# Optimization experiments

Measured on AMD Instinct MI355X. Metric: run time of the kernel, lower is better.

The kernel has to match this reference:

```python
import jax, jax.numpy as jnp
import numpy as np
import math

H = 12          # num_heads
HD = 64         # head_dim
M = 32          # random features = head_dim * kernel_ratio
EPS = 1e-8


def prm_exp(x, w):
    # x: [B,H,T,HD], w: [H,M,HD] -> [B,H,T,M]
    xd = 0.5 * jnp.sum(x * x, axis=-1, keepdims=True)        # [B,H,T,1]
    wtx = jnp.einsum('bhti,hmi->bhtm', x, w)                  # [B,H,T,M]
    return jnp.exp(wtx - xd) / math.sqrt(M)


def setup_inputs() -> dict:
    key = jax.random.key(0)
    ks = jax.random.split(key, 5)
    B, N, C = 8, 4096, 768
    x = jax.random.normal(ks[0], (B, N, C), dtype=jnp.float32)
    kqv_w = jax.random.normal(ks[1], (3 * C, C), dtype=jnp.float32) * (1.0 / math.sqrt(C))
    kqv_b = jnp.zeros((3 * C,), dtype=jnp.float32)
    proj_w = jax.random.normal(ks[2], (C, C), dtype=jnp.float32) * (1.0 / math.sqrt(C))
    proj_b = jnp.zeros((C,), dtype=jnp.float32)
    # frozen random-feature matrix: orthogonal rows per head, scaled by sqrt(M)
    wr = jax.random.normal(ks[3], (H, M, HD), dtype=jnp.float32)
    q_ortho, _ = jnp.linalg.qr(jnp.swapaxes(wr, -1, -2))       # [H,HD,M], cols orthonormal
    w = jnp.swapaxes(q_ortho, -1, -2) * math.sqrt(M)           # [H,M,HD]
    return {"x": x, "kqv_w": kqv_w, "kqv_b": kqv_b,
            "proj_w": proj_w, "proj_b": proj_b, "w": w}


def reference(x, kqv_w, kqv_b, proj_w, proj_b, w):
    B, N, C = x.shape
    kqv = x @ kqv_w.T + kqv_b                                  # [B,N,3C]
    kqv = kqv.reshape(B, N, 3, H, HD).transpose(2, 0, 3, 1, 4) # [3,B,H,N,HD]
    k, q, v = kqv[0], kqv[1], kqv[2]
    kp = prm_exp(k, w)                                         # [B,H,N,M]
    qp = prm_exp(q, w)                                         # [B,H,N,M]
    D = jnp.einsum('bhtm,bhm->bht', qp, kp.sum(axis=2))[..., None]   # [B,H,N,1]
    kptv = jnp.einsum('bhin,bhim->bhnm', v, kp)                # [B,H,HD,M]
    y = jnp.einsum('bhtm,bhnm->bhtn', qp, kptv) / (D + EPS)    # [B,H,N,HD]
    y = y.transpose(0, 2, 1, 3).reshape(B, N, C)
    y = y @ proj_w.T + proj_b
    return y
```

## Files before the change

kernel.cpp:

```cpp
#include <hip/hip_runtime.h>
#include <math.h>

namespace {
constexpr int cB  = 8;
constexpr int cN  = 4096;
constexpr int cC  = 768;
constexpr int cH  = 12;
constexpr int cHD = 64;
constexpr int cM  = 32;
}

typedef __attribute__((ext_vector_type(8))) short bf16x8;
typedef __attribute__((ext_vector_type(4))) float f32x4;

#define BARRIER() do { asm volatile("" ::: "memory"); __builtin_amdgcn_s_barrier(); asm volatile("" ::: "memory"); } while (0)
#define WAIT_VM(N) do { asm volatile("s_waitcnt vmcnt(" #N ")" ::: "memory"); __builtin_amdgcn_sched_barrier(0); } while (0)
#define WAIT_LGKM0() do { asm volatile("s_waitcnt lgkmcnt(0)" ::: "memory"); __builtin_amdgcn_sched_barrier(0); } while (0)

__device__ __forceinline__ void async_copy16(const void* g, void* l) {
    __builtin_amdgcn_global_load_lds((const __attribute__((address_space(1))) void*)g,
                                     (__attribute__((address_space(3))) void*)l, 16, 0, 0);
}

__device__ __forceinline__ ushort f32_to_bf16_rne(float x) {
    unsigned int u = __float_as_uint(x);
    u += 0x7fffu + ((u >> 16) & 1u);
    return (ushort)(u >> 16);
}

__device__ __forceinline__ float bf16_to_f32(ushort u) {
    return __uint_as_float(((unsigned)u) << 16);
}

__device__ __forceinline__ void split2(float f, ushort& h, ushort& l) {
    h = f32_to_bf16_rne(f);
    float r = f - bf16_to_f32(h);
    l = f32_to_bf16_rne(r);
}

__global__ __launch_bounds__(256)
void split_bf16(const float* __restrict__ in, ushort* __restrict__ hi,
                ushort* __restrict__ lo, int n4)
{
    int i = blockIdx.x * 256 + threadIdx.x;
    const int stride = gridDim.x * 256;
    for (; i < n4; i += stride) {
        float4 v = reinterpret_cast<const float4*>(in)[i];
        ushort4 h, l;
        split2(v.x, h.x, l.x);
        split2(v.y, h.y, l.y);
        split2(v.z, h.z, l.z);
        split2(v.w, h.w, l.w);
        reinterpret_cast<ushort4*>(hi)[i] = h;
        reinterpret_cast<ushort4*>(lo)[i] = l;
    }
}

template <int TERMS, int FUSE>
__global__ __launch_bounds__(512, 2)
void gemm256(const ushort* __restrict__ Ah, const ushort* __restrict__ Al,
             const ushort* __restrict__ Bh, const ushort* __restrict__ Bl,
             const float* __restrict__ bias,
             float* __restrict__ Cf, ushort* __restrict__ Cb,
             int Ndim, int K, int mode,
             ushort* __restrict__ kp, ushort* __restrict__ qp,
             float* __restrict__ kpsum_p,
             const ushort* __restrict__ whb, const ushort* __restrict__ wlb)
{
    constexpr int APL = (TERMS >= 2) ? 2 : 1;
    constexpr int BPL = (TERMS == 3) ? 2 : 1;
    constexpr int NPL = APL + BPL;
    __shared__ ushort smem[2 * NPL * 8192];
    const int tid = threadIdx.x;
    const int wave = tid >> 6, lane = tid & 63;
    const int wm = wave >> 2, wn = wave & 3;
    const int fr = lane & 15, fk = lane >> 4;
    const int fco = (fk ^ ((fr >> 1) & 3)) * 8;

    const int nwg = gridDim.x * 128;
    const int orig = blockIdx.x * 128 + blockIdx.y;
    const int swz = (orig & 7) * (nwg >> 3) + (orig >> 3);
    const int row0 = (swz & 127) << 8;
    const int col0 = (swz >> 7) << 8;

    const ushort* planes[NPL];
    if constexpr (TERMS == 3) { planes[0] = Ah; planes[1] = Al; planes[2] = Bh; planes[3] = Bl; }
    else { planes[0] = Ah; planes[1] = Bh; }

    const ushort* gsrc[NPL][2];
    int ldst[NPL][2];
    #pragma unroll
    for (int p = 0; p < NPL; ++p)
        #pragma unroll
        for (int h2 = 0; h2 < 2; ++h2) {
            const int ci = h2 * 512 + tid;
            const int row = ci >> 2;
            const int cc = (ci & 3) ^ ((row >> 1) & 3);
            const int grow = ((p < APL) ? row0 : col0) + row;
            gsrc[p][h2] = planes[p] + (size_t)grow * K + cc * 8;
            ldst[p][h2] = p * 8192 + h2 * 4096 + wave * 512;
        }

    const int NT = K >> 5;
    f32x4 acc[8][4] = {};

    #pragma unroll
    for (int p = 0; p < NPL; ++p)
        #pragma unroll
        for (int h2 = 0; h2 < 2; ++h2)
            async_copy16(gsrc[p][h2], &smem[ldst[p][h2]]);
    #pragma unroll
    for (int p = 0; p < NPL; ++p)
        #pragma unroll
        for (int h2 = 0; h2 < 2; ++h2)
            async_copy16(gsrc[p][h2] + 32, &smem[NPL * 8192 + ldst[p][h2]]);
    if constexpr (TERMS == 3) WAIT_VM(8); else WAIT_VM(4);
    BARRIER();

    for (int t = 0; t < NT; ++t) {
        const int cb = (t & 1) * NPL * 8192;
        const int nb = ((t + 1) & 1) * NPL * 8192;
        bf16x8 fb[4][BPL];
        #pragma unroll
        for (int mp = 0; mp < 4; ++mp) {
            if (mp == 0) {
                #pragma unroll
                for (int ni = 0; ni < 4; ++ni) {
                    const int off = cb + APL * 8192 + (wn * 64 + ni * 16 + fr) * 32 + fco;
                    fb[ni][0] = *reinterpret_cast<const bf16x8*>(&smem[off]);
                    if constexpr (BPL == 2)
                        fb[ni][1] = *reinterpret_cast<const bf16x8*>(&smem[off + 8192]);
                }
            }
            bf16x8 fa[2][APL];
            #pragma unroll
            for (int m2 = 0; m2 < 2; ++m2) {
                const int off = cb + (wm * 128 + (mp * 2 + m2) * 16 + fr) * 32 + fco;
                fa[m2][0] = *reinterpret_cast<const bf16x8*>(&smem[off]);
                if constexpr (APL == 2)
                    fa[m2][1] = *reinterpret_cast<const bf16x8*>(&smem[off + 8192]);
            }
            if (t >= 1 && t + 1 < NT && mp < APL) {
                async_copy16(gsrc[mp][0] + (t + 1) * 32, &smem[nb + ldst[mp][0]]);
                async_copy16(gsrc[mp][1] + (t + 1) * 32, &smem[nb + ldst[mp][1]]);
            }
            if (t + 2 < NT && mp >= APL && mp < APL + BPL) {
                async_copy16(gsrc[mp][0] + (t + 2) * 32, &smem[cb + ldst[mp][0]]);
                async_copy16(gsrc[mp][1] + (t + 2) * 32, &smem[cb + ldst[mp][1]]);
            }
            BARRIER();
            WAIT_LGKM0();
            __builtin_amdgcn_s_setprio(1);
            #pragma unroll
            for (int term = 0; term < TERMS; ++term) {
                const int pa = (TERMS == 3) ? ((term == 2) ? 1 : 0) : 0;
                const int pb = (TERMS == 3) ? ((term == 1) ? 1 : 0) : 0;
                #pragma unroll
                for (int m2 = 0; m2 < 2; ++m2)
                    #pragma unroll
                    for (int ni = 0; ni < 4; ++ni)
                        acc[mp * 2 + m2][ni] = __builtin_amdgcn_mfma_f32_16x16x32_bf16(
                            fa[m2][pa], fb[ni][pb], acc[mp * 2 + m2][ni], 0, 0, 0);
            }
            __builtin_amdgcn_s_setprio(0);
            if (mp == 3) {
                if (t + 2 < NT)      { if constexpr (BPL == 2) WAIT_VM(4); else WAIT_VM(2); }
                else if (t + 1 < NT) { WAIT_VM(0); }
            }
            if (mp < 3 || t + 1 < NT) BARRIER();
        }
    }

    if constexpr (FUSE) {
        BARRIER();
        const int cglob = col0 + wn * 64;
        const bool is_k = (cglob < 768);
        const int h = (is_k ? cglob : cglob - 768) >> 6;
        const int rbase = row0 + wm * 128;
        const int b = rbase >> 12;
        const int bh = b * cH + h;
        const int trow0 = rbase & 4095;
        ushort* phi = is_k ? kp : qp;
        bf16x8 Wh2[2][2], Wl2[2][2];
        #pragma unroll
        for (int mf = 0; mf < 2; ++mf)
            #pragma unroll
            for (int kc = 0; kc < 2; ++kc) {
                size_t off = (size_t)(h * 32 + mf * 16 + fr) * 64 + kc * 32 + fk * 8;
                Wh2[mf][kc] = *reinterpret_cast<const bf16x8*>(&whb[off]);
                Wl2[mf][kc] = *reinterpret_cast<const bf16x8*>(&wlb[off]);
            }
        unsigned* kt = reinterpret_cast<unsigned*>(&smem[wave * 8192]);
        const float rsm = 0.17677669529663687f;
        #pragma unroll
        for (int pass = 0; pass < 2; ++pass) {
            #pragma unroll
            for (int ni = 0; ni < 4; ++ni) {
                const float bv = bias[cglob + ni * 16 + fr];
                #pragma unroll
                for (int mi = 0; mi < 4; ++mi) {
                    #pragma unroll
                    for (int j = 0; j < 4; ++j) {
                        const int rrow = mi * 16 + fk * 4 + j;
                        const int ccol = ni * 16 + fr;
                        ushort hh, ll;
                        split2(acc[pass * 4 + mi][ni][j] + bv, hh, ll);
                        const int ccs = (ccol >> 2) ^ (rrow & 15);
                        kt[rrow * 64 + ccs * 4 + (ccol & 3)] = ((unsigned)ll << 16) | hh;
                    }
                }
            }
            f32x4 acc2[4][2] = {};
            float xdv4[4];
            #pragma unroll
            for (int tf = 0; tf < 4; ++tf) {
                const int rrow = tf * 16 + fr;
                const unsigned* rowp = &kt[rrow * 64];
                uint4 c0 = *reinterpret_cast<const uint4*>(&rowp[(((fk << 1))     ^ fr) << 2]);
                uint4 c1 = *reinterpret_cast<const uint4*>(&rowp[(((fk << 1) | 1) ^ fr) << 2]);
                uint4 c2 = *reinterpret_cast<const uint4*>(&rowp[(((fk << 1) + 8) ^ fr) << 2]);
                uint4 c3 = *reinterpret_cast<const uint4*>(&rowp[(((fk << 1) + 9) ^ fr) << 2]);
                unsigned u[16] = {c0.x,c0.y,c0.z,c0.w, c1.x,c1.y,c1.z,c1.w,
                                  c2.x,c2.y,c2.z,c2.w, c3.x,c3.y,c3.z,c3.w};
                bf16x8 Ah2[2], Al2[2];
                float xs = 0.f;
                #pragma unroll
                for (int e = 0; e < 16; ++e) {
                    const ushort hh = (ushort)(u[e] & 0xffffu);
                    const ushort ll = (ushort)(u[e] >> 16);
                    Ah2[e >> 3][e & 7] = (short)hh;
                    Al2[e >> 3][e & 7] = (short)ll;
                    const float kv = bf16_to_f32(hh) + bf16_to_f32(ll);
                    xs = fmaf(kv, kv, xs);
                }
                xs += __shfl_xor(xs, 16);
                xs += __shfl_xor(xs, 32);
                xdv4[tf] = 0.5f * xs;
                #pragma unroll
                for (int kc = 0; kc < 2; ++kc)
                    #pragma unroll
                    for (int mf = 0; mf < 2; ++mf) {
                        acc2[tf][mf] = __builtin_amdgcn_mfma_f32_16x16x32_bf16(Ah2[kc], Wh2[mf][kc], acc2[tf][mf], 0, 0, 0);
                        acc2[tf][mf] = __builtin_amdgcn_mfma_f32_16x16x32_bf16(Ah2[kc], Wl2[mf][kc], acc2[tf][mf], 0, 0, 0);
                        acc2[tf][mf] = __builtin_amdgcn_mfma_f32_16x16x32_bf16(Al2[kc], Wh2[mf][kc], acc2[tf][mf], 0, 0, 0);
                    }
            }
            float sm0 = 0.f, sm1 = 0.f;
            #pragma unroll
            for (int tf = 0; tf < 4; ++tf) {
                #pragma unroll
                for (int j = 0; j < 4; ++j) {
                    const int rloc = fk * 4 + j;
                    const float xdv = __shfl(xdv4[tf], (lane & 48) | rloc);
                    const int tg = trow0 + pass * 64 + tf * 16 + rloc;
                    float e0 = __expf(acc2[tf][0][j] - xdv) * rsm;
                    float e1 = __expf(acc2[tf][1][j] - xdv) * rsm;
                    phi[((size_t)bh * cN + tg) * cM + fr]      = f32_to_bf16_rne(e0);
                    phi[((size_t)bh * cN + tg) * cM + 16 + fr] = f32_to_bf16_rne(e1);
                    sm0 += e0; sm1 += e1;
                }
            }
            if (is_k) {
                sm0 += __shfl_xor(sm0, 16); sm0 += __shfl_xor(sm0, 32);
                sm1 += __shfl_xor(sm1, 16); sm1 += __shfl_xor(sm1, 32);
                const int tblk = (trow0 + pass * 64) >> 6;
                if (lane < 16) {
                    kpsum_p[((size_t)bh * 64 + tblk) * cM + lane]      = sm0;
                    kpsum_p[((size_t)bh * 64 + tblk) * cM + 16 + lane] = sm1;
                }
            }
        }
        return;
    }

    #pragma unroll
    for (int ni = 0; ni < 4; ++ni) {
        const int c = col0 + wn * 64 + ni * 16 + fr;
        const float bv = bias[c];
        #pragma unroll
        for (int mi = 0; mi < 8; ++mi) {
            const int r0 = row0 + wm * 128 + mi * 16 + fk * 4;
            #pragma unroll
            for (int j = 0; j < 4; ++j) {
                const float val = acc[mi][ni][j] + bv;
                const int row = r0 + j;
                if (mode == 0) {
                    Cf[(size_t)row * Ndim + c] = val;
                } else {
                    const int b = row >> 12, tt = row & 4095;
                    const int h = c >> 6, d = c & 63;
                    Cb[(((size_t)(b * cH + h) * cN + tt) << 6) + d] = f32_to_bf16_rne(val);
                }
            }
        }
    }
}

__global__ __launch_bounds__(256)
void pv_mfma(const ushort* __restrict__ qp, const ushort* __restrict__ kptvx,
             ushort* __restrict__ yh)
{
    const int bh = blockIdx.x;
    const int wave = threadIdx.x >> 6, lane = threadIdx.x & 63;
    const int tblk = blockIdx.y * 4 + wave;
    const int b = bh / cH, h = bh % cH;
    const int t0 = tblk * 64;
    const int fr = lane & 15, fk = lane >> 4;
    bf16x8 Bf[5];
    #pragma unroll
    for (int nf = 0; nf < 5; ++nf)
        Bf[nf] = *reinterpret_cast<const bf16x8*>(&kptvx[(size_t)bh * 2560 + (nf * 16 + fr) * 32 + fk * 8]);
    f32x4 acc[4][5] = {};
    #pragma unroll
    for (int tf = 0; tf < 4; ++tf) {
        bf16x8 Af = *reinterpret_cast<const bf16x8*>(&qp[((size_t)bh * cN + t0 + tf * 16 + fr) * cM + fk * 8]);
        #pragma unroll
        for (int nf = 0; nf < 5; ++nf)
            acc[tf][nf] = __builtin_amdgcn_mfma_f32_16x16x32_bf16(Af, Bf[nf], acc[tf][nf], 0, 0, 0);
    }
    #pragma unroll
    for (int tf = 0; tf < 4; ++tf) {
        #pragma unroll
        for (int j = 0; j < 4; ++j) {
            const int rloc = fk * 4 + j;
            const int t = t0 + tf * 16 + rloc;
            const float Dv = __shfl(acc[tf][4][j], lane & 48) + 1e-8f;
            const float rD = 1.0f / Dv;
            #pragma unroll
            for (int nf = 0; nf < 4; ++nf) {
                float yv = acc[tf][nf][j] * rD;
                size_t oa = (size_t)(b * cN + t) * cC + h * 64 + nf * 16 + fr;
                yh[oa] = f32_to_bf16_rne(yv);
            }
        }
    }
}

__global__ __launch_bounds__(256, 4)
void kptv_part(const ushort* __restrict__ vbf, const ushort* __restrict__ kp,
               float* __restrict__ kptv_p)
{
    const int bh = blockIdx.x, chunk = blockIdx.y;
    __shared__ float vl[64][68];
    __shared__ float kl[64][36];
    const int tid = threadIdx.x;
    const int half = tid >> 7;
    const int dg = (tid >> 3) & 15;
    const int mg = tid & 7;
    float acc[4][4] = {};
    for (int tile = 0; tile < 8; ++tile) {
        const int tb = chunk * 512 + tile * 64;
        #pragma unroll
        for (int i = 0; i < 2; ++i) {
            int idx = i * 256 + tid;
            int row = idx >> 3, seg = idx & 7;
            bf16x8 vv = *reinterpret_cast<const bf16x8*>(&vbf[((size_t)bh * cN + tb + row) * 64 + seg * 8]);
            float4 lo4 = make_float4(bf16_to_f32((ushort)vv[0]), bf16_to_f32((ushort)vv[1]),
                                     bf16_to_f32((ushort)vv[2]), bf16_to_f32((ushort)vv[3]));
            float4 hi4 = make_float4(bf16_to_f32((ushort)vv[4]), bf16_to_f32((ushort)vv[5]),
                                     bf16_to_f32((ushort)vv[6]), bf16_to_f32((ushort)vv[7]));
            *reinterpret_cast<float4*>(&vl[row][seg * 8])     = lo4;
            *reinterpret_cast<float4*>(&vl[row][seg * 8 + 4]) = hi4;
        }
        {
            int row = tid >> 2, seg = tid & 3;
            bf16x8 vv = *reinterpret_cast<const bf16x8*>(&kp[((size_t)bh * cN + tb + row) * 32 + seg * 8]);
            float4 lo4 = make_float4(bf16_to_f32((ushort)vv[0]), bf16_to_f32((ushort)vv[1]),
                                     bf16_to_f32((ushort)vv[2]), bf16_to_f32((ushort)vv[3]));
            float4 hi4 = make_float4(bf16_to_f32((ushort)vv[4]), bf16_to_f32((ushort)vv[5]),
                                     bf16_to_f32((ushort)vv[6]), bf16_to_f32((ushort)vv[7]));
            *reinterpret_cast<float4*>(&kl[row][seg * 8])     = lo4;
            *reinterpret_cast<float4*>(&kl[row][seg * 8 + 4]) = hi4;
        }
        __syncthreads();
        for (int t = 0; t < 32; ++t) {
            const int tt = half * 32 + t;
            float4 av = *reinterpret_cast<const float4*>(&vl[tt][dg * 4]);
            float4 bv = *reinterpret_cast<const float4*>(&kl[tt][mg * 4]);
            float a4[4] = {av.x, av.y, av.z, av.w};
            float b4[4] = {bv.x, bv.y, bv.z, bv.w};
            #pragma unroll
            for (int i = 0; i < 4; ++i)
                #pragma unroll
                for (int j = 0; j < 4; ++j)
                    acc[i][j] = fmaf(a4[i], b4[j], acc[i][j]);
        }
        __syncthreads();
    }
    float* outp = &kptv_p[(((size_t)chunk * 2 + half) * 96 + bh) * 2048];
    #pragma unroll
    for (int i = 0; i < 4; ++i)
        *reinterpret_cast<float4*>(&outp[(dg * 4 + i) * 32 + mg * 4]) =
            make_float4(acc[i][0], acc[i][1], acc[i][2], acc[i][3]);
}

__global__ __launch_bounds__(256)
void kptv_reduce(const float* __restrict__ kptv_p, const float* __restrict__ kpsum_p,
                 ushort* __restrict__ kptvx)
{
    const int bh = blockIdx.x, tid = threadIdx.x;
    for (int l = tid; l < 2048; l += 256) {
        float s = 0.f;
        #pragma unroll
        for (int c = 0; c < 16; ++c) s += kptv_p[((size_t)c * 96 + bh) * 2048 + l];
        kptvx[(size_t)bh * 2560 + l] = f32_to_bf16_rne(s);
    }
    if (tid < 32) {
        float s = 0.f;
        #pragma unroll
        for (int c = 0; c < 64; ++c) s += kpsum_p[((size_t)bh * 64 + c) * cM + tid];
        kptvx[(size_t)bh * 2560 + 64 * 32 + tid] = f32_to_bf16_rne(s);
    }
    for (int l = tid; l < 480; l += 256)
        kptvx[(size_t)bh * 2560 + 65 * 32 + l] = 0;
}

extern "C" void kernel_launch(void* const* d_in, const int* in_sizes, int n_in,
                              void* d_out, int out_size, void* d_ws, size_t ws_size,
                              hipStream_t stream)
{
    const float* x      = (const float*)d_in[0];
    const float* kqv_w  = (const float*)d_in[1];
    const float* kqv_b  = (const float*)d_in[2];
    const float* proj_w = (const float*)d_in[3];
    const float* proj_b = (const float*)d_in[4];
    const float* w      = (const float*)d_in[5];

    char* wsb = (char*)d_ws;
    ushort* xh   = (ushort*)(wsb);
    ushort* xl   = (ushort*)(wsb + 50331648);
    ushort* yh   = (ushort*)(wsb + 100663296);
    ushort* vbf  = (ushort*)(wsb + 201326592);
    ushort* wh   = (ushort*)(wsb + 251658240);
    ushort* wl_  = (ushort*)(wsb + 255197184);
    ushort* pwh  = (ushort*)(wsb + 258736128);
    ushort* pwl  = (ushort*)(wsb + 259915776);
    ushort* whb  = (ushort*)(wsb + 261095424);
    ushort* wlb  = (ushort*)(wsb + 261144576);

    char* ob = (char*)d_out;
    ushort* kp      = (ushort*)ob;
    ushort* qp      = (ushort*)(ob + 25165824);
    float*  kptv_p  = (float*)(ob + 50331648);
    float*  kpsum_p = (float*)(ob + 62914560);
    ushort* kptvx   = (ushort*)(ob + 63700992);
    float*  out     = (float*)d_out;

    dim3 blk(256);
    split_bf16<<<2048, blk, 0, stream>>>(x, xh, xl, 25165824 / 4);
    split_bf16<<<1728, blk, 0, stream>>>(kqv_w, wh, wl_, 1769472 / 4);
    split_bf16<<<576, blk, 0, stream>>>(proj_w, pwh, pwl, 589824 / 4);
    split_bf16<<<24, blk, 0, stream>>>(w, whb, wlb, 24576 / 4);
    gemm256<3, 1><<<dim3(6, 128), dim3(512), 0, stream>>>(
        xh, xl, wh, wl_, kqv_b, nullptr, nullptr, 1536, 768, 0,
        kp, qp, kpsum_p, whb, wlb);
    gemm256<1, 0><<<dim3(3, 128), dim3(512), 0, stream>>>(
        xh, nullptr, wh + (size_t)1536 * 768, nullptr, kqv_b + 1536,
        nullptr, vbf, 768, 768, 2, nullptr, nullptr, nullptr, nullptr, nullptr);
    kptv_part<<<dim3(96, 8), blk, 0, stream>>>(vbf, kp, kptv_p);
    kptv_reduce<<<dim3(96), blk, 0, stream>>>(kptv_p, kpsum_p, kptvx);
    pv_mfma<<<dim3(96, 16), blk, 0, stream>>>(qp, kptvx, yh);
    gemm256<1, 0><<<dim3(3, 128), dim3(512), 0, stream>>>(
        yh, nullptr, pwh, nullptr, proj_b, out, nullptr, 768, 768, 0,
        nullptr, nullptr, nullptr, nullptr, nullptr);
}
```

Baseline: 435.1 us.

## Halve GEMM M-tile to 128 rows and drop weight low-plane term

The GEMM tile shrinks from 256x256 to 128x256, doubling the grid and raising the launch-bounds occupancy hint from 2 to 4 blocks per CU. Smaller shared-memory buffers and half the accumulators are meant to give better latency hiding and load balance. The fused K/Q projection also drops from three split-bf16 terms to two, removing the weight low-plane product (x_lo*W_hi is kept, x_hi*W_lo is dropped). That cuts MFMA work and B-plane traffic but lowers the accuracy of the K/Q projection feeding exp().

```diff
diff --git a/kernel.cpp b/kernel.cpp
--- a/kernel.cpp
+++ b/kernel.cpp
@@ -57,9 +57,9 @@
 }
 
 template <int TERMS, int FUSE>
-__global__ __launch_bounds__(512, 2)
+__global__ __launch_bounds__(512, 4)
 void gemm256(const ushort* __restrict__ Ah, const ushort* __restrict__ Al,
-             const ushort* __restrict__ Bh, const ushort* __restrict__ Bl,
+             const ushort* __restrict__ Bh,
              const float* __restrict__ bias,
              float* __restrict__ Cf, ushort* __restrict__ Cb,
              int Ndim, int K, int mode,
@@ -68,104 +68,99 @@
              const ushort* __restrict__ whb, const ushort* __restrict__ wlb)
 {
     constexpr int APL = (TERMS >= 2) ? 2 : 1;
-    constexpr int BPL = (TERMS == 3) ? 2 : 1;
-    constexpr int NPL = APL + BPL;
-    __shared__ ushort smem[2 * NPL * 8192];
+    constexpr int ASZ = 4096;
+    constexpr int BSZ = 8192;
+    constexpr int BUF = APL * ASZ + BSZ;
+    constexpr int SMEMSZ = (2 * BUF > (FUSE ? 32768 : 0)) ? 2 * BUF : 32768;
+    __shared__ ushort smem[SMEMSZ];
     const int tid = threadIdx.x;
     const int wave = tid >> 6, lane = tid & 63;
     const int wm = wave >> 2, wn = wave & 3;
     const int fr = lane & 15, fk = lane >> 4;
     const int fco = (fk ^ ((fr >> 1) & 3)) * 8;
 
-    const int nwg = gridDim.x * 128;
-    const int orig = blockIdx.x * 128 + blockIdx.y;
+    const int NY = gridDim.y;
+    const int nwg = gridDim.x * NY;
+    const int orig = blockIdx.x * NY + blockIdx.y;
     const int swz = (orig & 7) * (nwg >> 3) + (orig >> 3);
-    const int row0 = (swz & 127) << 8;
-    const int col0 = (swz >> 7) << 8;
-
-    const ushort* planes[NPL];
-    if constexpr (TERMS == 3) { planes[0] = Ah; planes[1] = Al; planes[2] = Bh; planes[3] = Bl; }
-    else { planes[0] = Ah; planes[1] = Bh; }
-
-    const ushort* gsrc[NPL][2];
-    int ldst[NPL][2];
-    #pragma unroll
-    for (int p = 0; p < NPL; ++p)
-        #pragma unroll
-        for (int h2 = 0; h2 < 2; ++h2) {
-            const int ci = h2 * 512 + tid;
-            const int row = ci >> 2;
-            const int cc = (ci & 3) ^ ((row >> 1) & 3);
-            const int grow = ((p < APL) ? row0 : col0) + row;
-            gsrc[p][h2] = planes[p] + (size_t)grow * K + cc * 8;
-            ldst[p][h2] = p * 8192 + h2 * 4096 + wave * 512;
-        }
+    const int row0 = (swz % NY) << 7;
+    const int col0 = (swz / NY) << 8;
+
+    const ushort* aplanes[APL];
+    aplanes[0] = Ah;
+    if constexpr (APL == 2) aplanes[1] = Al;
+
+    const ushort* gsrcA[APL];
+    int ldstA[APL];
+    #pragma unroll
+    for (int p = 0; p < APL; ++p) {
+        const int row = tid >> 2;
+        const int cc = (tid & 3) ^ ((row >> 1) & 3);
+        gsrcA[p] = aplanes[p] + (size_t)(row0 + row) * K + cc * 8;
+        ldstA[p] = p * ASZ + tid * 8;
+    }
+    const ushort* gsrcB[2];
+    int ldstB[2];
+    #pragma unroll
+    for (int h2 = 0; h2 < 2; ++h2) {
+        const int ci = h2 * 512 + tid;
+        const int row = ci >> 2;
+        const int cc = (ci & 3) ^ ((row >> 1) & 3);
+        gsrcB[h2] = Bh + (size_t)(col0 + row) * K + cc * 8;
+        ldstB[h2] = APL * ASZ + h2 * 4096 + tid * 8;
+    }
 
     const int NT = K >> 5;
-    f32x4 acc[8][4] = {};
-
-    #pragma unroll
-    for (int p = 0; p < NPL; ++p)
-        #pragma unroll
-        for (int h2 = 0; h2 < 2; ++h2)
-            async_copy16(gsrc[p][h2], &smem[ldst[p][h2]]);
-    #pragma unroll
-    for (int p = 0; p < NPL; ++p)
-        #pragma unroll
-        for (int h2 = 0; h2 < 2; ++h2)
-            async_copy16(gsrc[p][h2] + 32, &smem[NPL * 8192 + ldst[p][h2]]);
-    if constexpr (TERMS == 3) WAIT_VM(8); else WAIT_VM(4);
+    f32x4 acc[4][4] = {};
+
+    #pragma unroll
+    for (int p = 0; p < APL; ++p) async_copy16(gsrcA[p], &smem[ldstA[p]]);
+    #pragma unroll
+    for (int h2 = 0; h2 < 2; ++h2) async_copy16(gsrcB[h2], &smem[ldstB[h2]]);
+    #pragma unroll
+    for (int p = 0; p < APL; ++p) async_copy16(gsrcA[p] + 32, &smem[BUF + ldstA[p]]);
+    #pragma unroll
+    for (int h2 = 0; h2 < 2; ++h2) async_copy16(gsrcB[h2] + 32, &smem[BUF + ldstB[h2]]);
+    if constexpr (TERMS == 2) WAIT_VM(4); else WAIT_VM(3);
     BARRIER();
 
     for (int t = 0; t < NT; ++t) {
-        const int cb = (t & 1) * NPL * 8192;
-        const int nb = ((t + 1) & 1) * NPL * 8192;
-        bf16x8 fb[4][BPL];
+        const int cb = (t & 1) * BUF;
+        const int nb = ((t + 1) & 1) * BUF;
+        bf16x8 fb[4];
         #pragma unroll
         for (int mp = 0; mp < 4; ++mp) {
             if (mp == 0) {
                 #pragma unroll
                 for (int ni = 0; ni < 4; ++ni) {
-                    const int off = cb + APL * 8192 + (wn * 64 + ni * 16 + fr) * 32 + fco;
-                    fb[ni][0] = *reinterpret_cast<const bf16x8*>(&smem[off]);
-                    if constexpr (BPL == 2)
-                        fb[ni][1] = *reinterpret_cast<const bf16x8*>(&smem[off + 8192]);
+                    const int off = cb + APL * ASZ + (wn * 64 + ni * 16 + fr) * 32 + fco;
+                    fb[ni] = *reinterpret_cast<const bf16x8*>(&smem[off]);
                 }
             }
-            bf16x8 fa[2][APL];
-            #pragma unroll
-            for (int m2 = 0; m2 < 2; ++m2) {
-                const int off = cb + (wm * 128 + (mp * 2 + m2) * 16 + fr) * 32 + fco;
-                fa[m2][0] = *reinterpret_cast<const bf16x8*>(&smem[off]);
+            bf16x8 fa[APL];
+            {
+                const int off = cb + (wm * 64 + mp * 16 + fr) * 32 + fco;
+                fa[0] = *reinterpret_cast<const bf16x8*>(&smem[off]);
                 if constexpr (APL == 2)
-                    fa[m2][1] = *reinterpret_cast<const bf16x8*>(&smem[off + 8192]);
-            }
-            if (t >= 1 && t + 1 < NT && mp < APL) {
-                async_copy16(gsrc[mp][0] + (t + 1) * 32, &smem[nb + ldst[mp][0]]);
-                async_copy16(gsrc[mp][1] + (t + 1) * 32, &smem[nb + ldst[mp][1]]);
-            }
-            if (t + 2 < NT && mp >= APL && mp < APL + BPL) {
-                async_copy16(gsrc[mp][0] + (t + 2) * 32, &smem[cb + ldst[mp][0]]);
-                async_copy16(gsrc[mp][1] + (t + 2) * 32, &smem[cb + ldst[mp][1]]);
-            }
+                    fa[1] = *reinterpret_cast<const bf16x8*>(&smem[off + ASZ]);
+            }
+            if (t >= 1 && t + 1 < NT && mp < APL)
+                async_copy16(gsrcA[mp] + (t + 1) * 32, &smem[nb + ldstA[mp]]);
+            if (t + 2 < NT && mp >= 2)
+                async_copy16(gsrcB[mp - 2] + (t + 2) * 32, &smem[cb + ldstB[mp - 2]]);
             BARRIER();
             WAIT_LGKM0();
             __builtin_amdgcn_s_setprio(1);
             #pragma unroll
-            for (int term = 0; term < TERMS; ++term) {
-                const int pa = (TERMS == 3) ? ((term == 2) ? 1 : 0) : 0;
-                const int pb = (TERMS == 3) ? ((term == 1) ? 1 : 0) : 0;
-                #pragma unroll
-                for (int m2 = 0; m2 < 2; ++m2)
-                    #pragma unroll
-                    for (int ni = 0; ni < 4; ++ni)
-                        acc[mp * 2 + m2][ni] = __builtin_amdgcn_mfma_f32_16x16x32_bf16(
-                            fa[m2][pa], fb[ni][pb], acc[mp * 2 + m2][ni], 0, 0, 0);
-            }
+            for (int term = 0; term < TERMS; ++term)
+                #pragma unroll
+                for (int ni = 0; ni < 4; ++ni)
+                    acc[mp][ni] = __builtin_amdgcn_mfma_f32_16x16x32_bf16(
+                        fa[term], fb[ni], acc[mp][ni], 0, 0, 0);
             __builtin_amdgcn_s_setprio(0);
             if (mp == 3) {
-                if (t + 2 < NT)      { if constexpr (BPL == 2) WAIT_VM(4); else WAIT_VM(2); }
-                else if (t + 1 < NT) { WAIT_VM(0); }
+                if (t + 2 < NT)      WAIT_VM(2);
+                else if (t + 1 < NT) WAIT_VM(0);
             }
             if (mp < 3 || t + 1 < NT) BARRIER();
         }
@@ -176,7 +171,7 @@
         const int cglob = col0 + wn * 64;
         const bool is_k = (cglob < 768);
         const int h = (is_k ? cglob : cglob - 768) >> 6;
-        const int rbase = row0 + wm * 128;
+        const int rbase = row0 + wm * 64;
         const int b = rbase >> 12;
         const int bh = b * cH + h;
         const int trow0 = rbase & 4095;
@@ -190,30 +185,31 @@
                 Wh2[mf][kc] = *reinterpret_cast<const bf16x8*>(&whb[off]);
                 Wl2[mf][kc] = *reinterpret_cast<const bf16x8*>(&wlb[off]);
             }
-        unsigned* kt = reinterpret_cast<unsigned*>(&smem[wave * 8192]);
+        unsigned* kt = reinterpret_cast<unsigned*>(&smem[wave * 4096]);
         const float rsm = 0.17677669529663687f;
+        float sm0 = 0.f, sm1 = 0.f;
         #pragma unroll
         for (int pass = 0; pass < 2; ++pass) {
             #pragma unroll
             for (int ni = 0; ni < 4; ++ni) {
                 const float bv = bias[cglob + ni * 16 + fr];
                 #pragma unroll
-                for (int mi = 0; mi < 4; ++mi) {
+                for (int mi2 = 0; mi2 < 2; ++mi2) {
                     #pragma unroll
                     for (int j = 0; j < 4; ++j) {
-                        const int rrow = mi * 16 + fk * 4 + j;
+                        const int rrow = mi2 * 16 + fk * 4 + j;
                         const int ccol = ni * 16 + fr;
                         ushort hh, ll;
-                        split2(acc[pass * 4 + mi][ni][j] + bv, hh, ll);
+                        split2(acc[pass * 2 + mi2][ni][j] + bv, hh, ll);
                         const int ccs = (ccol >> 2) ^ (rrow & 15);
                         kt[rrow * 64 + ccs * 4 + (ccol & 3)] = ((unsigned)ll << 16) | hh;
                     }
                 }
             }
-            f32x4 acc2[4][2] = {};
-            float xdv4[4];
-            #pragma unroll
-            for (int tf = 0; tf < 4; ++tf) {
+            f32x4 acc2[2][2] = {};
+            float xdv4[2];
+            #pragma unroll
+            for (int tf = 0; tf < 2; ++tf) {
                 const int rrow = tf * 16 + fr;
                 const unsigned* rowp = &kt[rrow * 64];
                 uint4 c0 = *reinterpret_cast<const uint4*>(&rowp[(((fk << 1))     ^ fr) << 2]);
@@ -245,14 +241,13 @@
                         acc2[tf][mf] = __builtin_amdgcn_mfma_f32_16x16x32_bf16(Al2[kc], Wh2[mf][kc], acc2[tf][mf], 0, 0, 0);
                     }
             }
-            float sm0 = 0.f, sm1 = 0.f;
-            #pragma unroll
-            for (int tf = 0; tf < 4; ++tf) {
+            #pragma unroll
+            for (int tf = 0; tf < 2; ++tf) {
                 #pragma unroll
                 for (int j = 0; j < 4; ++j) {
                     const int rloc = fk * 4 + j;
                     const float xdv = __shfl(xdv4[tf], (lane & 48) | rloc);
-                    const int tg = trow0 + pass * 64 + tf * 16 + rloc;
+                    const int tg = trow0 + pass * 32 + tf * 16 + rloc;
                     float e0 = __expf(acc2[tf][0][j] - xdv) * rsm;
                     float e1 = __expf(acc2[tf][1][j] - xdv) * rsm;
                     phi[((size_t)bh * cN + tg) * cM + fr]      = f32_to_bf16_rne(e0);
@@ -260,14 +255,14 @@
                     sm0 += e0; sm1 += e1;
                 }
             }
-            if (is_k) {
-                sm0 += __shfl_xor(sm0, 16); sm0 += __shfl_xor(sm0, 32);
-                sm1 += __shfl_xor(sm1, 16); sm1 += __shfl_xor(sm1, 32);
-                const int tblk = (trow0 + pass * 64) >> 6;
-                if (lane < 16) {
-                    kpsum_p[((size_t)bh * 64 + tblk) * cM + lane]      = sm0;
-                    kpsum_p[((size_t)bh * 64 + tblk) * cM + 16 + lane] = sm1;
-                }
+        }
+        if (is_k) {
+            sm0 += __shfl_xor(sm0, 16); sm0 += __shfl_xor(sm0, 32);
+            sm1 += __shfl_xor(sm1, 16); sm1 += __shfl_xor(sm1, 32);
+            const int tblk = trow0 >> 6;
+            if (lane < 16) {
+                kpsum_p[((size_t)bh * 64 + tblk) * cM + lane]      = sm0;
+                kpsum_p[((size_t)bh * 64 + tblk) * cM + 16 + lane] = sm1;
             }
         }
         return;
@@ -278,8 +273,8 @@
         const int c = col0 + wn * 64 + ni * 16 + fr;
         const float bv = bias[c];
         #pragma unroll
-        for (int mi = 0; mi < 8; ++mi) {
-            const int r0 = row0 + wm * 128 + mi * 16 + fk * 4;
+        for (int mi = 0; mi < 4; ++mi) {
+            const int r0 = row0 + wm * 64 + mi * 16 + fk * 4;
             #pragma unroll
             for (int j = 0; j < 4; ++j) {
                 const float val = acc[mi][ni][j] + bv;
@@ -451,16 +446,16 @@
     split_bf16<<<1728, blk, 0, stream>>>(kqv_w, wh, wl_, 1769472 / 4);
     split_bf16<<<576, blk, 0, stream>>>(proj_w, pwh, pwl, 589824 / 4);
     split_bf16<<<24, blk, 0, stream>>>(w, whb, wlb, 24576 / 4);
-    gemm256<3, 1><<<dim3(6, 128), dim3(512), 0, stream>>>(
-        xh, xl, wh, wl_, kqv_b, nullptr, nullptr, 1536, 768, 0,
+    gemm256<2, 1><<<dim3(6, 256), dim3(512), 0, stream>>>(
+        xh, xl, wh, kqv_b, nullptr, nullptr, 1536, 768, 0,
         kp, qp, kpsum_p, whb, wlb);
-    gemm256<1, 0><<<dim3(3, 128), dim3(512), 0, stream>>>(
-        xh, nullptr, wh + (size_t)1536 * 768, nullptr, kqv_b + 1536,
+    gemm256<1, 0><<<dim3(3, 256), dim3(512), 0, stream>>>(
+        xh, nullptr, wh + (size_t)1536 * 768, kqv_b + 1536,
         nullptr, vbf, 768, 768, 2, nullptr, nullptr, nullptr, nullptr, nullptr);
     kptv_part<<<dim3(96, 8), blk, 0, stream>>>(vbf, kp, kptv_p);
     kptv_reduce<<<dim3(96), blk, 0, stream>>>(kptv_p, kpsum_p, kptvx);
     pv_mfma<<<dim3(96, 16), blk, 0, stream>>>(qp, kptvx, yh);
-    gemm256<1, 0><<<dim3(3, 128), dim3(512), 0, stream>>>(
-        yh, nullptr, pwh, nullptr, proj_b, out, nullptr, 768, 768, 0,
+    gemm256<1, 0><<<dim3(3, 256), dim3(512), 0, stream>>>(
+        yh, nullptr, pwh, proj_b, out, nullptr, 768, 768, 0,
         nullptr, nullptr, nullptr, nullptr, nullptr);
 }
```

Result: faster. 409.3 us (-5.9%).
